# Kernel optimization log

Hardware: AMD Instinct MI355X
Metric: run time of the kernel (lower is better)

## Reference

```python
import jax, jax.numpy as jnp
import numpy as np
import math

D_MODEL = 1024
D_STATE = 16
D_CONV = 4
EXPAND = 2
D_INNER = EXPAND * D_MODEL
BATCH = 8
SEQ_LEN = 2048
DT_MIN, DT_MAX = 1e-3, 1e-1


def setup_inputs() -> dict:
    key = jax.random.key(0)
    ks = jax.random.split(key, 8)
    scale = 0.02
    x = jax.random.normal(ks[0], (BATCH, SEQ_LEN, D_MODEL), dtype=jnp.float32)
    W_in = jax.random.normal(ks[1], (2 * D_INNER, D_MODEL), dtype=jnp.float32) * scale
    conv_w = jax.random.normal(ks[2], (D_INNER, 1, D_CONV), dtype=jnp.float32) * scale  # depthwise [O,I/g,K]
    conv_b = jnp.zeros((D_INNER,), dtype=jnp.float32)
    W_x = jax.random.normal(ks[3], (2 * D_STATE + 1, D_INNER), dtype=jnp.float32) * scale
    W_dt = jax.random.normal(ks[4], (D_INNER, 1), dtype=jnp.float32) * scale
    # dt bias init: softplus^{-1}(dt) with dt ~ LogUniform(dt_min, dt_max)
    u = jax.random.uniform(ks[5], (D_INNER,), dtype=jnp.float32)
    dt = jnp.clip(jnp.exp(u * (math.log(DT_MAX) - math.log(DT_MIN)) + math.log(DT_MIN)), DT_MIN, None)
    b_dt = dt + jnp.log(-jnp.expm1(-dt))
    # A_log = log(A), A[d,n] = n+1
    A_log = jnp.log(jnp.broadcast_to(jnp.arange(1, D_STATE + 1, dtype=jnp.float32), (D_INNER, D_STATE)))
    D = jnp.ones((D_INNER,), dtype=jnp.float32)
    W_out = jax.random.normal(ks[6], (D_MODEL, D_INNER), dtype=jnp.float32) * scale
    return {"x": x, "W_in": W_in, "conv_w": conv_w, "conv_b": conv_b,
            "W_x": W_x, "W_dt": W_dt, "b_dt": b_dt, "A_log": A_log, "D": D, "W_out": W_out}


def _selective_ssm(xs, W_x, W_dt, b_dt, A_log, D):
    # xs: [B, L, Di]
    B_, L, Di = xs.shape
    N = A_log.shape[1]
    A = -jnp.exp(A_log)  # [Di, N]
    x_dbl = xs @ W_x.T  # [B, L, 2N+1]
    dt_raw, Bm, Cm = jnp.split(x_dbl, [1, 1 + N], axis=-1)
    dt = jax.nn.softplus(dt_raw @ W_dt.T + b_dt)  # [B, L, Di]

    def step(h, inp):
        dt_t, B_t, C_t, x_t = inp  # [B,Di], [B,N], [B,N], [B,Di]
        A_bar = jnp.exp(dt_t[..., None] * A)                      # [B, Di, N]
        h = A_bar * h + (dt_t * x_t)[..., None] * B_t[:, None, :]  # [B, Di, N]
        y_t = jnp.einsum('bdn,bn->bd', h, C_t)
        return h, y_t

    h0 = jnp.zeros((B_, Di, N), dtype=xs.dtype)
    inps = (jnp.moveaxis(dt, 1, 0), jnp.moveaxis(Bm, 1, 0),
            jnp.moveaxis(Cm, 1, 0), jnp.moveaxis(xs, 1, 0))
    _, ys = jax.lax.scan(step, h0, inps)  # ys: [L, B, Di]
    return jnp.moveaxis(ys, 0, 1) + D * xs


def reference(x, W_in, conv_w, conv_b, W_x, W_dt, b_dt, A_log, D, W_out):
    B_, L, _ = x.shape
    xz = x @ W_in.T  # [B, L, 2*Di]
    xi, z = jnp.split(xz, 2, axis=-1)
    # causal depthwise conv1d (torch pads both sides by d_conv-1 then slices [:L] == left pad)
    xc = jnp.transpose(xi, (0, 2, 1))  # [B, Di, L]
    xc = jax.lax.conv_general_dilated(
        xc, conv_w, window_strides=(1,), padding=[(conv_w.shape[-1] - 1, 0)],
        dimension_numbers=('NCH', 'OIH', 'NCH'), feature_group_count=conv_w.shape[0])
    xc = xc + conv_b[None, :, None]
    xs = jax.nn.silu(jnp.transpose(xc, (0, 2, 1)))  # [B, L, Di]
    y = _selective_ssm(xs, W_x, W_dt, b_dt, A_log, D)
    out = (y * jax.nn.silu(z)) @ W_out.T  # [B, L, d_model]
    return out
```

## Files before the change

### kernel.cpp

```cpp
#include <hip/hip_runtime.h>
#include <math.h>

#define BB    8
#define LL    2048
#define DMOD  1024
#define DI    2048
#define NST   16
#define MR    (BB*LL)
#define NCH   16
#define CLEN  128
#define XDW   36

typedef unsigned short bf16_t;
typedef __attribute__((ext_vector_type(8))) __bf16 bf16x8;
typedef __attribute__((ext_vector_type(4))) float  f32x4;

__device__ __forceinline__ float b2f(bf16_t u) {
  return __uint_as_float(((unsigned int)u) << 16);
}
__device__ __forceinline__ bf16_t f2bn(float f) {
  __bf16 h = (__bf16)f;
  return *(bf16_t*)&h;
}

__device__ __forceinline__ void cstore(float* p, float v)  { *p = v; }
__device__ __forceinline__ void cstore(bf16_t* p, float v) { *p = f2bn(v); }

__device__ __forceinline__ void gld16(const bf16_t* g, bf16_t* l) {
  __builtin_amdgcn_global_load_lds(
      (const __attribute__((address_space(1))) unsigned int*)g,
      (__attribute__((address_space(3))) unsigned int*)l, 16, 0, 0);
}

__device__ __forceinline__ float softplus(float x) {
  return (x > 20.f) ? x : __logf(1.f + __expf(x));
}
__device__ __forceinline__ float silu(float z) {
  return z * __builtin_amdgcn_rcpf(1.f + __expf(-z));
}

__global__ __launch_bounds__(256) void cvt_bf16(
    const float* __restrict__ in, bf16_t* __restrict__ out, int n4)
{
  int i = blockIdx.x * 256 + threadIdx.x;
  if (i >= n4) return;
  float4 v = ((const float4*)in)[i];
  ushort4 u;
  u.x = f2bn(v.x); u.y = f2bn(v.y); u.z = f2bn(v.z); u.w = f2bn(v.w);
  ((ushort4*)out)[i] = u;
}

__global__ __launch_bounds__(256) void cvt_wx(
    const float* __restrict__ W_x, bf16_t* __restrict__ Wx_bf)
{
  int i = blockIdx.x * 256 + threadIdx.x;
  int j = i >> 11;
  Wx_bf[i] = (j < 33) ? f2bn(W_x[i]) : (bf16_t)0;
}

template <typename TC>
__global__ __launch_bounds__(512) void mgemm_big(
    const bf16_t* __restrict__ A, const bf16_t* __restrict__ B,
    TC* __restrict__ C, int N, int K)
{
  __shared__ __align__(16) bf16_t As[3][256 * 32];
  __shared__ __align__(16) bf16_t Bs[3][256 * 32];
  const int tid  = threadIdx.x;
  const int wave = tid >> 6;
  const int lane = tid & 63;
  const int m0 = blockIdx.y * 256;
  const int n0 = blockIdx.x * 256;
  const int fr = lane & 15;
  const int quad = lane >> 4;
  const int wm = (wave >> 2) * 128;
  const int wn = (wave & 3) * 64;

  const int srow = tid >> 2;
  const int schk = tid & 3;
  const int ssw  = schk ^ ((srow >> 1) & 3);
  const bf16_t* Ag = A + (size_t)(m0 + srow) * K + ssw * 8;
  const bf16_t* Bg = B + (size_t)(n0 + srow) * K + ssw * 8;
  const size_t r128 = (size_t)128 * K;

  int aoff[8], boff[4];
#pragma unroll
  for (int i = 0; i < 8; ++i) {
    int row = wm + i * 16 + fr;
    aoff[i] = row * 32 + ((quad ^ ((row >> 1) & 3)) * 8);
  }
#pragma unroll
  for (int j = 0; j < 4; ++j) {
    int row = wn + j * 16 + fr;
    boff[j] = row * 32 + ((quad ^ ((row >> 1) & 3)) * 8);
  }

  f32x4 acc[8][4];
#pragma unroll
  for (int i = 0; i < 8; ++i)
#pragma unroll
    for (int j = 0; j < 4; ++j) acc[i][j] = (f32x4){0.f, 0.f, 0.f, 0.f};

  const int nkt = K >> 5;
  gld16(Ag,            &As[0][wave * 512]);
  gld16(Ag + r128,     &As[0][4096 + wave * 512]);
  gld16(Bg,            &Bs[0][wave * 512]);
  gld16(Bg + r128,     &Bs[0][4096 + wave * 512]);
  gld16(Ag + 32,       &As[1][wave * 512]);
  gld16(Ag + r128 + 32,&As[1][4096 + wave * 512]);
  gld16(Bg + 32,       &Bs[1][wave * 512]);
  gld16(Bg + r128 + 32,&Bs[1][4096 + wave * 512]);
  asm volatile("s_waitcnt vmcnt(4)\n\ts_barrier" ::: "memory");

  for (int t = 0; t < nkt; ++t) {
    const int p = t % 3;
    if (t + 2 < nkt) {
      const int p2 = (t + 2) % 3;
      const size_t ko = (size_t)(t + 2) * 32;
      gld16(Ag + ko,        &As[p2][wave * 512]);
      gld16(Ag + r128 + ko, &As[p2][4096 + wave * 512]);
      gld16(Bg + ko,        &Bs[p2][wave * 512]);
      gld16(Bg + r128 + ko, &Bs[p2][4096 + wave * 512]);
    }
    const bf16_t* Ab = &As[p][0];
    const bf16_t* Bb = &Bs[p][0];
    bf16x8 a[8], b[4];
#pragma unroll
    for (int i = 0; i < 8; ++i) a[i] = *(const bf16x8*)&Ab[aoff[i]];
#pragma unroll
    for (int j = 0; j < 4; ++j) b[j] = *(const bf16x8*)&Bb[boff[j]];
    __builtin_amdgcn_s_setprio(1);
#pragma unroll
    for (int i = 0; i < 8; ++i)
#pragma unroll
      for (int j = 0; j < 4; ++j)
        acc[i][j] = __builtin_amdgcn_mfma_f32_16x16x32_bf16(a[i], b[j], acc[i][j], 0, 0, 0);
    __builtin_amdgcn_s_setprio(0);
    if (t + 2 < nkt) {
      asm volatile("s_waitcnt vmcnt(4)\n\ts_barrier" ::: "memory");
    } else if (t + 1 < nkt) {
      asm volatile("s_waitcnt vmcnt(0)\n\ts_barrier" ::: "memory");
    }
  }

#pragma unroll
  for (int i = 0; i < 8; ++i)
#pragma unroll
    for (int j = 0; j < 4; ++j) {
#pragma unroll
      for (int r = 0; r < 4; ++r) {
        int grow = m0 + wm + i * 16 + quad * 4 + r;
        int gcol = n0 + wn + j * 16 + fr;
        cstore(&C[(size_t)grow * N + gcol], acc[i][j][r]);
      }
    }
}

__global__ __launch_bounds__(256) void xdbl_mfma(
    const bf16_t* __restrict__ xs, const bf16_t* __restrict__ Wx_bf,
    float* __restrict__ xdbl)
{
  __shared__ __align__(16) bf16_t As[2 * 64 * 32];
  __shared__ __align__(16) bf16_t Bs[2 * 64 * 32];
  const int tid  = threadIdx.x;
  const int wave = tid >> 6;
  const int lane = tid & 63;
  const int m0 = blockIdx.x * 64;
  const int fr = lane & 15;
  const int quad = lane >> 4;

  const int srow = wave * 16 + (lane >> 2);
  const int scol = (lane & 3) * 8;
  const bf16_t* Ag = xs + (size_t)(m0 + srow) * DI + scol;
  const bf16_t* Bg = Wx_bf + (size_t)srow * DI + scol;
  bf16_t* lA = As + wave * 512;
  bf16_t* lB = Bs + wave * 512;

  f32x4 acc[3];
#pragma unroll
  for (int jt = 0; jt < 3; ++jt) acc[jt] = (f32x4){0.f, 0.f, 0.f, 0.f};

  for (int k0 = 0; k0 < DI; k0 += 64) {
    __syncthreads();
#pragma unroll
    for (int kk = 0; kk < 2; ++kk) {
      gld16(Ag + k0 + kk * 32, lA + kk * 2048);
      gld16(Bg + k0 + kk * 32, lB + kk * 2048);
    }
    __syncthreads();

#pragma unroll
    for (int kk = 0; kk < 2; ++kk) {
      bf16x8 a = *(const bf16x8*)&As[kk * 2048 + (wave * 16 + fr) * 32 + quad * 8];
#pragma unroll
      for (int jt = 0; jt < 3; ++jt) {
        bf16x8 b = *(const bf16x8*)&Bs[kk * 2048 + (jt * 16 + fr) * 32 + quad * 8];
        acc[jt] = __builtin_amdgcn_mfma_f32_16x16x32_bf16(a, b, acc[jt], 0, 0, 0);
      }
    }
  }

#pragma unroll
  for (int jt = 0; jt < 3; ++jt) {
#pragma unroll
    for (int r = 0; r < 4; ++r) {
      int grow = m0 + wave * 16 + quad * 4 + r;
      int j = jt * 16 + fr;
      if (j < 33) {
        int col = (j == 0) ? 0 : (j + 3);
        xdbl[(size_t)grow * XDW + col] = acc[jt][r];
      }
    }
  }
}

__global__ __launch_bounds__(256) void conv_silu(
    const bf16_t* __restrict__ xz, const float* __restrict__ cw,
    const float* __restrict__ cb, bf16_t* __restrict__ xs)
{
  int idx = blockIdx.x * 256 + threadIdx.x;
  int d4 = idx & 511;
  int l  = (idx >> 9) & 2047;
  int b  = idx >> 20;
  int d  = d4 * 4;

  float wch[4][4];
#pragma unroll
  for (int c = 0; c < 4; ++c)
#pragma unroll
    for (int k = 0; k < 4; ++k) wch[c][k] = cw[(d + c) * 4 + k];

  float acc0 = cb[d+0], acc1 = cb[d+1], acc2 = cb[d+2], acc3 = cb[d+3];
  size_t rowbase = ((size_t)b * LL + l) * 4096 + d;
#pragma unroll
  for (int k = 0; k < 4; ++k) {
    if (l - 3 + k >= 0) {
      ushort4 u = *(const ushort4*)(xz + rowbase - (size_t)(3 - k) * 4096);
      acc0 += b2f(u.x) * wch[0][k];
      acc1 += b2f(u.y) * wch[1][k];
      acc2 += b2f(u.z) * wch[2][k];
      acc3 += b2f(u.w) * wch[3][k];
    }
  }
  ushort4 o;
  o.x = f2bn(silu(acc0)); o.y = f2bn(silu(acc1));
  o.z = f2bn(silu(acc2)); o.w = f2bn(silu(acc3));
  *(ushort4*)(xs + ((size_t)b * LL + l) * (size_t)DI + d) = o;
}

__global__ __launch_bounds__(256) void scan_pass1(
    const float* __restrict__ xdbl, const bf16_t* __restrict__ xs,
    const float* __restrict__ W_dt, const float* __restrict__ b_dt,
    const float* __restrict__ A_log, float* __restrict__ states)
{
  const int bid = blockIdx.x;
  const int dg = bid & 7, c = (bid >> 3) & 15, b = bid >> 7;
  const int d = dg * 256 + threadIdx.x;

  const float A2_0 = -__expf(A_log[(size_t)d * NST]) * 1.44269504f;
  bool ok = true;
#pragma unroll
  for (int n = 1; n < NST; ++n) {
    float a = -__expf(A_log[(size_t)d * NST + n]) * 1.44269504f;
    ok = ok && (fabsf(a - (float)(n + 1) * A2_0) <= 1e-3f * (float)(n + 1));
  }
  __shared__ int s_ok;
  __shared__ float sx[64 * XDW];
  if (threadIdx.x == 0) s_ok = 1;
  __syncthreads();
  if (!ok) s_ok = 0;
  __syncthreads();
  const bool fast = (s_ok != 0);

  float h[NST];
#pragma unroll
  for (int n = 0; n < NST; ++n) h[n] = 0.f;
  const float wdt = W_dt[d], bdt = b_dt[d];
  float dts = 0.f;
  const size_t rbase = (size_t)b * LL + c * CLEN;
  float xv = b2f(xs[rbase * DI + d]);

  if (fast) {
    for (int s = 0; s < CLEN; s += 64) {
      __syncthreads();
      const float* xg = xdbl + (rbase + s) * XDW;
      for (int q = threadIdx.x; q < 64 * XDW; q += 256) sx[q] = xg[q];
      __syncthreads();
#pragma unroll 2
      for (int u = 0; u < 64; ++u) {
        int tn = s + u + 1;
        float nx = 0.f;
        if (tn < CLEN) nx = b2f(xs[(rbase + tn) * DI + d]);
        float dtr = sx[u * XDW];
        float dt = softplus(fmaf(dtr, wdt, bdt));
        dts += dt;
        float dx = dt * xv;
        float wv[NST];
        wv[0] = exp2f(dt * A2_0);
#pragma unroll
        for (int n = 1; n < NST; ++n)
          wv[n] = wv[(n - 1) >> 1] * wv[n - 1 - ((n - 1) >> 1)];
        const float4* Bp = (const float4*)&sx[u * XDW + 4];
#pragma unroll
        for (int n4 = 0; n4 < 4; ++n4) {
          float4 Bv = Bp[n4];
          float bb[4] = {Bv.x, Bv.y, Bv.z, Bv.w};
#pragma unroll
          for (int k = 0; k < 4; ++k) {
            int n = n4 * 4 + k;
            h[n] = fmaf(wv[n], h[n], dx * bb[k]);
          }
        }
        xv = nx;
      }
    }
    size_t sb = (((size_t)b * NCH + c) * DI + d) * 32;
    float Wv[NST];
    Wv[0] = exp2f(dts * A2_0);
#pragma unroll
    for (int n = 1; n < NST; ++n)
      Wv[n] = Wv[(n - 1) >> 1] * Wv[n - 1 - ((n - 1) >> 1)];
#pragma unroll
    for (int n = 0; n < NST; ++n) {
      states[sb + n]      = Wv[n];
      states[sb + 16 + n] = h[n];
    }
  } else {
    float A2[NST];
#pragma unroll
    for (int n = 0; n < NST; ++n)
      A2[n] = -__expf(A_log[(size_t)d * NST + n]) * 1.44269504f;
    for (int s = 0; s < CLEN; s += 64) {
      __syncthreads();
      const float* xg = xdbl + (rbase + s) * XDW;
      for (int q = threadIdx.x; q < 64 * XDW; q += 256) sx[q] = xg[q];
      __syncthreads();
#pragma unroll 2
      for (int u = 0; u < 64; ++u) {
        int tn = s + u + 1;
        float nx = 0.f;
        if (tn < CLEN) nx = b2f(xs[(rbase + tn) * DI + d]);
        float dtr = sx[u * XDW];
        float dt = softplus(fmaf(dtr, wdt, bdt));
        dts += dt;
        float dx = dt * xv;
        const float4* Bp = (const float4*)&sx[u * XDW + 4];
#pragma unroll
        for (int n4 = 0; n4 < 4; ++n4) {
          float4 Bv = Bp[n4];
          float bb[4] = {Bv.x, Bv.y, Bv.z, Bv.w};
#pragma unroll
          for (int k = 0; k < 4; ++k) {
            int n = n4 * 4 + k;
            h[n] = fmaf(exp2f(dt * A2[n]), h[n], dx * bb[k]);
          }
        }
        xv = nx;
      }
    }
    size_t sb = (((size_t)b * NCH + c) * DI + d) * 32;
#pragma unroll
    for (int n = 0; n < NST; ++n) {
      states[sb + n]      = exp2f(dts * A2[n]);
      states[sb + 16 + n] = h[n];
    }
  }
}

__global__ __launch_bounds__(256) void scan_pass2(float* __restrict__ states)
{
  int t = blockIdx.x * 256 + threadIdx.x;
  int n = t & 15, d = (t >> 4) & 2047, b = t >> 15;
  float h = 0.f;
  for (int c = 0; c < NCH; ++c) {
    size_t sb = (((size_t)b * NCH + c) * DI + d) * 32;
    float P  = states[sb + n];
    float h0 = states[sb + 16 + n];
    states[sb + n] = h;
    h = fmaf(P, h, h0);
  }
}

__global__ __launch_bounds__(256) void scan_pass3(
    const float* __restrict__ xdbl, const bf16_t* __restrict__ xz,
    bf16_t* __restrict__ xs, const float* __restrict__ states,
    const float* __restrict__ W_dt, const float* __restrict__ b_dt,
    const float* __restrict__ A_log, const float* __restrict__ Dp)
{
  const int bid = blockIdx.x;
  const int dg = bid & 7, c = (bid >> 3) & 15, b = bid >> 7;
  const int d = dg * 256 + threadIdx.x;

  const float A2_0 = -__expf(A_log[(size_t)d * NST]) * 1.44269504f;
  bool ok = true;
#pragma unroll
  for (int n = 1; n < NST; ++n) {
    float a = -__expf(A_log[(size_t)d * NST + n]) * 1.44269504f;
    ok = ok && (fabsf(a - (float)(n + 1) * A2_0) <= 1e-3f * (float)(n + 1));
  }
  __shared__ int s_ok;
  __shared__ float sx[64 * XDW];
  if (threadIdx.x == 0) s_ok = 1;
  __syncthreads();
  if (!ok) s_ok = 0;
  __syncthreads();
  const bool fast = (s_ok != 0);

  float h[NST];
  size_t sb = (((size_t)b * NCH + c) * DI + d) * 32;
#pragma unroll
  for (int n = 0; n < NST; ++n) h[n] = states[sb + n];
  const float wdt = W_dt[d], bdt = b_dt[d];
  const float Dd = Dp[d];
  const size_t rbase = (size_t)b * LL + c * CLEN;

  float xv = b2f(xs[rbase * DI + d]);
  float zv = b2f(xz[rbase * 4096 + DI + d]);

  if (fast) {
    for (int s = 0; s < CLEN; s += 64) {
      __syncthreads();
      const float* xg = xdbl + (rbase + s) * XDW;
      for (int q = threadIdx.x; q < 64 * XDW; q += 256) sx[q] = xg[q];
      __syncthreads();
#pragma unroll 2
      for (int u = 0; u < 64; ++u) {
        size_t r = rbase + s + u;
        int tn = s + u + 1;
        float nx = 0.f, nz = 0.f;
        if (tn < CLEN) {
          nx = b2f(xs[(rbase + tn) * DI + d]);
          nz = b2f(xz[(rbase + tn) * 4096 + DI + d]);
        }
        float dtr = sx[u * XDW];
        float dt = softplus(fmaf(dtr, wdt, bdt));
        float dx = dt * xv;
        float y = Dd * xv;
        float wv[NST];
        wv[0] = exp2f(dt * A2_0);
#pragma unroll
        for (int n = 1; n < NST; ++n)
          wv[n] = wv[(n - 1) >> 1] * wv[n - 1 - ((n - 1) >> 1)];
        const float4* Bp = (const float4*)&sx[u * XDW + 4];
        const float4* Cp = (const float4*)&sx[u * XDW + 20];
#pragma unroll
        for (int n4 = 0; n4 < 4; ++n4) {
          float4 Bv = Bp[n4];
          float4 Cv = Cp[n4];
          float bb[4] = {Bv.x, Bv.y, Bv.z, Bv.w};
          float cc[4] = {Cv.x, Cv.y, Cv.z, Cv.w};
#pragma unroll
          for (int k = 0; k < 4; ++k) {
            int n = n4 * 4 + k;
            h[n] = fmaf(wv[n], h[n], dx * bb[k]);
            y = fmaf(h[n], cc[k], y);
          }
        }
        xs[r * DI + d] = f2bn(y * silu(zv));
        xv = nx; zv = nz;
      }
    }
  } else {
    float A2[NST];
#pragma unroll
    for (int n = 0; n < NST; ++n)
      A2[n] = -__expf(A_log[(size_t)d * NST + n]) * 1.44269504f;
    for (int s = 0; s < CLEN; s += 64) {
      __syncthreads();
      const float* xg = xdbl + (rbase + s) * XDW;
      for (int q = threadIdx.x; q < 64 * XDW; q += 256) sx[q] = xg[q];
      __syncthreads();
#pragma unroll 2
      for (int u = 0; u < 64; ++u) {
        size_t r = rbase + s + u;
        int tn = s + u + 1;
        float nx = 0.f, nz = 0.f;
        if (tn < CLEN) {
          nx = b2f(xs[(rbase + tn) * DI + d]);
          nz = b2f(xz[(rbase + tn) * 4096 + DI + d]);
        }
        float dtr = sx[u * XDW];
        float dt = softplus(fmaf(dtr, wdt, bdt));
        float dx = dt * xv;
        float y = Dd * xv;
        const float4* Bp = (const float4*)&sx[u * XDW + 4];
        const float4* Cp = (const float4*)&sx[u * XDW + 20];
#pragma unroll
        for (int n4 = 0; n4 < 4; ++n4) {
          float4 Bv = Bp[n4];
          float4 Cv = Cp[n4];
          float bb[4] = {Bv.x, Bv.y, Bv.z, Bv.w};
          float cc[4] = {Cv.x, Cv.y, Cv.z, Cv.w};
#pragma unroll
          for (int k = 0; k < 4; ++k) {
            int n = n4 * 4 + k;
            h[n] = fmaf(exp2f(dt * A2[n]), h[n], dx * bb[k]);
            y = fmaf(h[n], cc[k], y);
          }
        }
        xs[r * DI + d] = f2bn(y * silu(zv));
        xv = nx; zv = nz;
      }
    }
  }
}

extern "C" void kernel_launch(void* const* d_in, const int* in_sizes, int n_in,
                              void* d_out, int out_size, void* d_ws, size_t ws_size,
                              hipStream_t stream)
{
  const float* x     = (const float*)d_in[0];
  const float* W_in  = (const float*)d_in[1];
  const float* cw    = (const float*)d_in[2];
  const float* cb    = (const float*)d_in[3];
  const float* W_x   = (const float*)d_in[4];
  const float* W_dt  = (const float*)d_in[5];
  const float* b_dt  = (const float*)d_in[6];
  const float* A_log = (const float*)d_in[7];
  const float* Dp    = (const float*)d_in[8];
  const float* W_out = (const float*)d_in[9];
  float* out = (float*)d_out;

  bf16_t* xz = (bf16_t*)d_ws;
  bf16_t* xs = xz + (size_t)MR * 4096;

  bf16_t* x_bf    = (bf16_t*)d_out;
  bf16_t* Win_bf  = x_bf + (size_t)MR * DMOD;
  bf16_t* Wx_bf   = Win_bf + (size_t)4096 * DMOD;
  float*  states  = (float*)d_out;
  float*  xdbl    = states + (size_t)BB * NCH * DI * 32;
  bf16_t* Wout_bf = xz;

  cvt_bf16<<<(MR*DMOD/4 + 255)/256, 256, 0, stream>>>(x, x_bf, MR*DMOD/4);
  cvt_bf16<<<(4096*DMOD/4 + 255)/256, 256, 0, stream>>>(W_in, Win_bf, 4096*DMOD/4);
  cvt_wx<<<(64*DI)/256, 256, 0, stream>>>(W_x, Wx_bf);
  mgemm_big<bf16_t><<<dim3(4096/256, MR/256), 512, 0, stream>>>(x_bf, Win_bf, xz, 4096, DMOD);
  conv_silu<<<(BB*LL*512)/256, 256, 0, stream>>>(xz, cw, cb, xs);
  xdbl_mfma<<<MR/64, 256, 0, stream>>>(xs, Wx_bf, xdbl);
  scan_pass1<<<BB*NCH*8, 256, 0, stream>>>(xdbl, xs, W_dt, b_dt, A_log, states);
  scan_pass2<<<(BB*DI*NST)/256, 256, 0, stream>>>(states);
  scan_pass3<<<BB*NCH*8, 256, 0, stream>>>(xdbl, xz, xs, states, W_dt, b_dt, A_log, Dp);
  cvt_bf16<<<(DMOD*DI/4 + 255)/256, 256, 0, stream>>>(W_out, Wout_bf, DMOD*DI/4);
  mgemm_big<float><<<dim3(DMOD/256, MR/256), 512, 0, stream>>>(xs, Wout_bf, out, DMOD, DI);
}
```

Baseline: 720.1 us.

## Software-pipeline GEMM main loop with split A fragments and interleaved loads

Restructures the big bf16 GEMM main loop so each k-tile is processed in two halves. LDS fragment reads for the next half and global-to-LDS staging of future tiles are interleaved with the MFMA blocks, using explicit barriers and waitcnt, instead of loading all fragments and then running every MFMA. The aim is to hide LDS read latency and global loads behind matrix math. The cost is more barriers, higher register pressure from double fragment sets, and fragile hand-written synchronisation.

```diff
diff --git a/kernel.cpp b/kernel.cpp
--- a/kernel.cpp
+++ b/kernel.cpp
@@ -59,12 +59,11 @@
 }
 
 template <typename TC>
-__global__ __launch_bounds__(512) void mgemm_big(
+__global__ __launch_bounds__(512) void mgemm_p3(
     const bf16_t* __restrict__ A, const bf16_t* __restrict__ B,
     TC* __restrict__ C, int N, int K)
 {
-  __shared__ __align__(16) bf16_t As[3][256 * 32];
-  __shared__ __align__(16) bf16_t Bs[3][256 * 32];
+  __shared__ __align__(16) bf16_t lds[49152];
   const int tid  = threadIdx.x;
   const int wave = tid >> 6;
   const int lane = tid & 63;
@@ -76,10 +75,9 @@
   const int wn = (wave & 3) * 64;
 
   const int srow = tid >> 2;
-  const int schk = tid & 3;
-  const int ssw  = schk ^ ((srow >> 1) & 3);
-  const bf16_t* Ag = A + (size_t)(m0 + srow) * K + ssw * 8;
-  const bf16_t* Bg = B + (size_t)(n0 + srow) * K + ssw * 8;
+  const int ssw  = (tid & 3) ^ ((srow >> 1) & 3);
+  const bf16_t* Asrc = A + (size_t)(m0 + srow) * K + ssw * 8;
+  const bf16_t* Bsrc = B + (size_t)(n0 + srow) * K + ssw * 8;
   const size_t r128 = (size_t)128 * K;
 
   int aoff[8], boff[4];
@@ -94,52 +92,83 @@
     boff[j] = row * 32 + ((quad ^ ((row >> 1) & 3)) * 8);
   }
 
+#define AB_(u) (((u) % 3) * 8192)
+#define BB_(u) (24576 + ((u) % 3) * 8192)
+#define STAGE_A(u) do {                                                    \
+    const bf16_t* s_ = Asrc + (size_t)(u) * 32;                            \
+    bf16_t* l_ = lds + AB_(u) + wave * 512;                                \
+    gld16(s_, l_); gld16(s_ + r128, l_ + 4096);                            \
+  } while (0)
+#define STAGE_B(u) do {                                                    \
+    const bf16_t* s_ = Bsrc + (size_t)(u) * 32;                            \
+    bf16_t* l_ = lds + BB_(u) + wave * 512;                                \
+    gld16(s_, l_); gld16(s_ + r128, l_ + 4096);                            \
+  } while (0)
+#define LDA4(dst,u,ib) do {                                                \
+    const bf16_t* r_ = lds + AB_(u);                                       \
+    _Pragma("unroll")                                                      \
+    for (int i_ = 0; i_ < 4; ++i_)                                         \
+      dst[i_] = *(const bf16x8*)&r_[aoff[(ib) + i_]];                      \
+  } while (0)
+#define LDB4(dst,u) do {                                                   \
+    const bf16_t* r_ = lds + BB_(u);                                       \
+    _Pragma("unroll")                                                      \
+    for (int j_ = 0; j_ < 4; ++j_)                                         \
+      dst[j_] = *(const bf16x8*)&r_[boff[j_]];                             \
+  } while (0)
+#define MM16(ar,br,ib) do {                                                \
+    __builtin_amdgcn_s_setprio(1);                                         \
+    _Pragma("unroll")                                                      \
+    for (int i_ = 0; i_ < 4; ++i_)                                         \
+      _Pragma("unroll")                                                    \
+      for (int j_ = 0; j_ < 4; ++j_)                                       \
+        acc[(ib) + i_][j_] = __builtin_amdgcn_mfma_f32_16x16x32_bf16(      \
+            ar[i_], br[j_], acc[(ib) + i_][j_], 0, 0, 0);                  \
+    __builtin_amdgcn_s_setprio(0);                                         \
+  } while (0)
+#define BAR()   __builtin_amdgcn_s_barrier()
+#define LGKM0() do { asm volatile("s_waitcnt lgkmcnt(0)" ::: "memory");    \
+                     __builtin_amdgcn_sched_barrier(0); } while (0)
+#define VMBAR(n) asm volatile("s_waitcnt vmcnt(" #n ")\n\ts_barrier" ::: "memory")
+
   f32x4 acc[8][4];
 #pragma unroll
   for (int i = 0; i < 8; ++i)
 #pragma unroll
     for (int j = 0; j < 4; ++j) acc[i][j] = (f32x4){0.f, 0.f, 0.f, 0.f};
 
-  const int nkt = K >> 5;
-  gld16(Ag,            &As[0][wave * 512]);
-  gld16(Ag + r128,     &As[0][4096 + wave * 512]);
-  gld16(Bg,            &Bs[0][wave * 512]);
-  gld16(Bg + r128,     &Bs[0][4096 + wave * 512]);
-  gld16(Ag + 32,       &As[1][wave * 512]);
-  gld16(Ag + r128 + 32,&As[1][4096 + wave * 512]);
-  gld16(Bg + 32,       &Bs[1][wave * 512]);
-  gld16(Bg + r128 + 32,&Bs[1][4096 + wave * 512]);
-  asm volatile("s_waitcnt vmcnt(4)\n\ts_barrier" ::: "memory");
-
-  for (int t = 0; t < nkt; ++t) {
-    const int p = t % 3;
-    if (t + 2 < nkt) {
-      const int p2 = (t + 2) % 3;
-      const size_t ko = (size_t)(t + 2) * 32;
-      gld16(Ag + ko,        &As[p2][wave * 512]);
-      gld16(Ag + r128 + ko, &As[p2][4096 + wave * 512]);
-      gld16(Bg + ko,        &Bs[p2][wave * 512]);
-      gld16(Bg + r128 + ko, &Bs[p2][4096 + wave * 512]);
-    }
-    const bf16_t* Ab = &As[p][0];
-    const bf16_t* Bb = &Bs[p][0];
-    bf16x8 a[8], b[4];
-#pragma unroll
-    for (int i = 0; i < 8; ++i) a[i] = *(const bf16x8*)&Ab[aoff[i]];
-#pragma unroll
-    for (int j = 0; j < 4; ++j) b[j] = *(const bf16x8*)&Bb[boff[j]];
-    __builtin_amdgcn_s_setprio(1);
-#pragma unroll
-    for (int i = 0; i < 8; ++i)
-#pragma unroll
-      for (int j = 0; j < 4; ++j)
-        acc[i][j] = __builtin_amdgcn_mfma_f32_16x16x32_bf16(a[i], b[j], acc[i][j], 0, 0, 0);
-    __builtin_amdgcn_s_setprio(0);
-    if (t + 2 < nkt) {
-      asm volatile("s_waitcnt vmcnt(4)\n\ts_barrier" ::: "memory");
-    } else if (t + 1 < nkt) {
-      asm volatile("s_waitcnt vmcnt(0)\n\ts_barrier" ::: "memory");
-    }
+  bf16x8 aC0[4], aQ0[4], bC0[4], aC1[4], aQ1[4], bC1[4];
+
+  const int nu = K >> 5;
+
+  STAGE_B(0); STAGE_A(0); STAGE_B(1); STAGE_A(1);
+  VMBAR(4);
+  LDA4(aC0, 0, 0); LDB4(bC0, 0);
+  STAGE_B(2);
+  BAR(); LGKM0(); BAR();
+
+  for (int u = 0; u < nu; u += 2) {
+    const bool s2 = (u + 2 < nu), s3 = (u + 3 < nu), s4 = (u + 4 < nu);
+    LDA4(aQ0, u, 4);
+    if (s2) STAGE_A(u + 2);
+    BAR(); LGKM0();
+    MM16(aC0, bC0, 0);
+    if (s2) VMBAR(4); else VMBAR(0);
+    LDA4(aC1, u + 1, 0); LDB4(bC1, u + 1);
+    if (s3) STAGE_B(u + 3);
+    BAR(); LGKM0();
+    MM16(aQ0, bC0, 4);
+    BAR();
+    LDA4(aQ1, u + 1, 4);
+    if (s3) STAGE_A(u + 3);
+    BAR(); LGKM0();
+    MM16(aC1, bC1, 0);
+    if (s3) VMBAR(4); else VMBAR(0);
+    if (s2) { LDA4(aC0, u + 2, 0); LDB4(bC0, u + 2); }
+    if (s4) STAGE_B(u + 4);
+    BAR(); LGKM0();
+    MM16(aQ1, bC1, 4);
+    BAR();
   }
 
 #pragma unroll
@@ -153,6 +182,16 @@
         cstore(&C[(size_t)grow * N + gcol], acc[i][j][r]);
       }
     }
+#undef AB_
+#undef BB_
+#undef STAGE_A
+#undef STAGE_B
+#undef LDA4
+#undef LDB4
+#undef MM16
+#undef BAR
+#undef LGKM0
+#undef VMBAR
 }
 
 __global__ __launch_bounds__(256) void xdbl_mfma(
@@ -533,12 +572,12 @@
   cvt_bf16<<<(MR*DMOD/4 + 255)/256, 256, 0, stream>>>(x, x_bf, MR*DMOD/4);
   cvt_bf16<<<(4096*DMOD/4 + 255)/256, 256, 0, stream>>>(W_in, Win_bf, 4096*DMOD/4);
   cvt_wx<<<(64*DI)/256, 256, 0, stream>>>(W_x, Wx_bf);
-  mgemm_big<bf16_t><<<dim3(4096/256, MR/256), 512, 0, stream>>>(x_bf, Win_bf, xz, 4096, DMOD);
+  mgemm_p3<bf16_t><<<dim3(4096/256, MR/256), 512, 0, stream>>>(x_bf, Win_bf, xz, 4096, DMOD);
   conv_silu<<<(BB*LL*512)/256, 256, 0, stream>>>(xz, cw, cb, xs);
   xdbl_mfma<<<MR/64, 256, 0, stream>>>(xs, Wx_bf, xdbl);
   scan_pass1<<<BB*NCH*8, 256, 0, stream>>>(xdbl, xs, W_dt, b_dt, A_log, states);
   scan_pass2<<<(BB*DI*NST)/256, 256, 0, stream>>>(states);
   scan_pass3<<<BB*NCH*8, 256, 0, stream>>>(xdbl, xz, xs, states, W_dt, b_dt, A_log, Dp);
   cvt_bf16<<<(DMOD*DI/4 + 255)/256, 256, 0, stream>>>(W_out, Wout_bf, DMOD*DI/4);
-  mgemm_big<float><<<dim3(DMOD/256, MR/256), 512, 0, stream>>>(xs, Wout_bf, out, DMOD, DI);
-}
+  mgemm_p3<float><<<dim3(DMOD/256, MR/256), 512, 0, stream>>>(xs, Wout_bf, out, DMOD, DI);
+}
```

New measurement: 695.0 us. 3.5% less time.
